# Optimization experiments

Measured on AMD Instinct MI355X. Metric: run time of the kernel, lower is better.

The kernel has to match this reference:

```python
import jax, jax.numpy as jnp
import numpy as np

B, T, D = 4096, 64, 128  # batch, n_tokens, d_model
LN_EPS = 1e-5


def setup_inputs() -> dict:
    key = jax.random.key(0)
    ks = jax.random.split(key, 3)
    X = jax.random.normal(ks[0], (B, T, D), dtype=jnp.float32)
    # torch Linear weights are (out_features, in_features)
    W1 = jax.random.normal(ks[1], (D, T * D), dtype=jnp.float32) * (T * D) ** -0.5
    b1 = jnp.zeros((D,), dtype=jnp.float32)
    W2 = jax.random.normal(ks[2], (T * D, D), dtype=jnp.float32) * D ** -0.5
    b2 = jnp.zeros((T * D,), dtype=jnp.float32)
    gamma = jnp.ones((D,), dtype=jnp.float32)
    beta = jnp.zeros((D,), dtype=jnp.float32)
    return {"X": X, "W1": W1, "b1": b1, "W2": W2, "b2": b2, "gamma": gamma, "beta": beta}


def reference(X, W1, b1, W2, b2, gamma, beta):
    b, t, d = X.shape
    scale = d ** -0.5
    # single-head self-attention with Q=K=V=X
    scores = jnp.einsum("btd,bsd->bts", X, X) * scale          # (B,T,T)
    attn = jax.nn.softmax(scores, axis=-1)
    X_dot = jnp.einsum("bts,bsd->btd", attn, X)                 # (B,T,D)
    # deep MLP over flattened tokens
    Xf = X.reshape(b, t * d)
    h = jax.nn.relu(Xf @ W1.T + b1)                             # (B,D)
    X_deep = (h @ W2.T + b2).reshape(b, t, d)                   # (B,T,D)
    # residual + LayerNorm over last dim
    y = X_dot + X_deep + X
    mu = jnp.mean(y, axis=-1, keepdims=True)
    var = jnp.mean(jnp.square(y - mu), axis=-1, keepdims=True)
    y_hat = (y - mu) * jax.lax.rsqrt(var + LN_EPS)
    return y_hat * gamma + beta
```

## Files before the change

kernel.cpp:

```cpp
#include <hip/hip_runtime.h>

#define NB 4096
#define NT 64
#define ND 128
#define NTD 8192

using bf16x8 = __attribute__((ext_vector_type(8))) short;
using s16x4  = __attribute__((ext_vector_type(4))) short;
using f32x4  = __attribute__((ext_vector_type(4))) float;

__device__ __forceinline__ short f2bf(float x) {
  union { float f; unsigned u; } v; v.f = x;
  unsigned r = (v.u + 0x7FFFu + ((v.u >> 16) & 1u)) >> 16;
  return (short)r;
}
__device__ __forceinline__ float bf2f(short h) {
  union { unsigned u; float f; } v; v.u = ((unsigned)(unsigned short)h) << 16;
  return v.f;
}

__global__ __launch_bounds__(256) void k_cvt(const float* __restrict__ W1,
                                             const float* __restrict__ W2,
                                             short* __restrict__ W1b,
                                             short* __restrict__ W2b) {
  int idx = blockIdx.x * 256 + threadIdx.x;
  const float4* src; short* dst;
  if (idx < 262144) { src = (const float4*)W1; dst = W1b; }
  else { idx -= 262144; src = (const float4*)W2; dst = W2b; }
  float4 v = src[idx];
  s16x4 p = { f2bf(v.x), f2bf(v.y), f2bf(v.z), f2bf(v.w) };
  *(s16x4*)&dst[4 * idx] = p;
}

#define LDX 136
#define LDT 72
#define LDP 72

__global__ __launch_bounds__(256) void k_attn(const float* __restrict__ X,
                                              short* __restrict__ ydot) {
  __shared__ short Xl[NT * LDX];
  __shared__ short XT[ND * LDT];
  __shared__ short Pl[4][16 * LDP];

  const int b = blockIdx.x;
  const int tid = threadIdx.x;
  const float4* X4 = (const float4*)(X + (size_t)b * NTD);

  for (int it = 0; it < 8; ++it) {
    int idx = tid + 256 * it;
    int r = idx >> 5;
    int c4 = idx & 31;
    float4 v = X4[idx];
    short h0 = f2bf(v.x), h1 = f2bf(v.y), h2 = f2bf(v.z), h3 = f2bf(v.w);
    s16x4 p = { h0, h1, h2, h3 };
    *(s16x4*)&Xl[r * LDX + 4 * c4] = p;
    int c = 4 * c4;
    XT[(c + 0) * LDT + r] = h0;
    XT[(c + 1) * LDT + r] = h1;
    XT[(c + 2) * LDT + r] = h2;
    XT[(c + 3) * LDT + r] = h3;
  }
  __syncthreads();

  const int w = tid >> 6;
  const int l = tid & 63;
  const int g = l >> 4;
  const int ln = l & 15;

  f32x4 S[4];
  for (int tj = 0; tj < 4; ++tj) S[tj] = f32x4{0.f, 0.f, 0.f, 0.f};
  for (int kk = 0; kk < 4; ++kk) {
    bf16x8 a = *(const bf16x8*)&Xl[(16 * w + ln) * LDX + 32 * kk + 8 * g];
    for (int tj = 0; tj < 4; ++tj) {
      bf16x8 bb = *(const bf16x8*)&Xl[(16 * tj + ln) * LDX + 32 * kk + 8 * g];
      S[tj] = __builtin_amdgcn_mfma_f32_16x16x32_bf16(a, bb, S[tj], 0, 0, 0);
    }
  }

  const float scale = 0.08838834764831845f;
  float li[4];
  for (int i = 0; i < 4; ++i) {
    float p[4];
    float mx = -1e30f;
    for (int tj = 0; tj < 4; ++tj) {
      float s = S[tj][i] * scale;
      p[tj] = s;
      mx = fmaxf(mx, s);
    }
    for (int msk = 1; msk < 16; msk <<= 1) mx = fmaxf(mx, __shfl_xor(mx, msk));
    float sum = 0.f;
    for (int tj = 0; tj < 4; ++tj) {
      float e = __expf(p[tj] - mx);
      p[tj] = e;
      sum += e;
    }
    for (int msk = 1; msk < 16; msk <<= 1) sum += __shfl_xor(sum, msk);
    li[i] = 1.0f / sum;
    for (int tj = 0; tj < 4; ++tj)
      Pl[w][(4 * g + i) * LDP + 16 * tj + ln] = f2bf(p[tj]);
  }
  __syncthreads();

  bf16x8 a0 = *(const bf16x8*)&Pl[w][ln * LDP + 8 * g];
  bf16x8 a1 = *(const bf16x8*)&Pl[w][ln * LDP + 32 + 8 * g];
  short* yrow = ydot + (size_t)b * NTD;
  for (int c = 0; c < 8; ++c) {
    f32x4 acc = f32x4{0.f, 0.f, 0.f, 0.f};
    bf16x8 b0 = *(const bf16x8*)&XT[(16 * c + ln) * LDT + 8 * g];
    bf16x8 b1 = *(const bf16x8*)&XT[(16 * c + ln) * LDT + 32 + 8 * g];
    acc = __builtin_amdgcn_mfma_f32_16x16x32_bf16(a0, b0, acc, 0, 0, 0);
    acc = __builtin_amdgcn_mfma_f32_16x16x32_bf16(a1, b1, acc, 0, 0, 0);
    for (int i = 0; i < 4; ++i) {
      int row = 16 * w + 4 * g + i;
      int col = 16 * c + ln;
      float y = acc[i] * li[i] + bf2f(Xl[row * LDX + col]);
      yrow[row * ND + col] = f2bf(y);
    }
  }
}

#define LDA1 40

__global__ __launch_bounds__(256) void k_gemm1(const float* __restrict__ X,
                                               const short* __restrict__ W1b,
                                               float* __restrict__ hacc) {
  __shared__ short Al[64 * LDA1];
  __shared__ short Bl[128 * LDA1];
  const int mt = blockIdx.x;
  const int kz = blockIdx.y;
  const int tid = threadIdx.x;
  const int w = tid >> 6, l = tid & 63, g = l >> 4, ln = l & 15;

  f32x4 acc[8];
  for (int c = 0; c < 8; ++c) acc[c] = f32x4{0.f, 0.f, 0.f, 0.f};

  for (int s = 0; s < 16; ++s) {
    int kb = kz * 512 + s * 32;
    for (int it = 0; it < 2; ++it) {
      int idx = tid + 256 * it;
      int r = idx >> 3, f = idx & 7;
      float4 v = ((const float4*)X)[(size_t)(mt * 64 + r) * 2048 + (kb >> 2) + f];
      s16x4 p = { f2bf(v.x), f2bf(v.y), f2bf(v.z), f2bf(v.w) };
      *(s16x4*)&Al[r * LDA1 + 4 * f] = p;
    }
    for (int it = 0; it < 2; ++it) {
      int idx = tid + 256 * it;
      int n = idx >> 2, f = idx & 3;
      bf16x8 v = *(const bf16x8*)&W1b[(size_t)n * NTD + kb + 8 * f];
      *(bf16x8*)&Bl[n * LDA1 + 8 * f] = v;
    }
    __syncthreads();
    bf16x8 a = *(const bf16x8*)&Al[(16 * w + ln) * LDA1 + 8 * g];
    for (int c = 0; c < 8; ++c) {
      bf16x8 bb = *(const bf16x8*)&Bl[(16 * c + ln) * LDA1 + 8 * g];
      acc[c] = __builtin_amdgcn_mfma_f32_16x16x32_bf16(a, bb, acc[c], 0, 0, 0);
    }
    __syncthreads();
  }
  for (int c = 0; c < 8; ++c)
    for (int i = 0; i < 4; ++i) {
      int m = mt * 64 + 16 * w + 4 * g + i;
      int n = 16 * c + ln;
      atomicAdd(&hacc[m * ND + n], acc[c][i]);
    }
}

__global__ __launch_bounds__(256) void k_hact(const float* __restrict__ hacc,
                                              const float* __restrict__ b1,
                                              short* __restrict__ hb) {
  int idx = blockIdx.x * 256 + threadIdx.x;
  float v = hacc[idx] + b1[idx & 127];
  hb[idx] = f2bf(fmaxf(v, 0.f));
}

#define LDK 136

__global__ __launch_bounds__(256) void k_gemm2(const short* __restrict__ hb,
                                               const short* __restrict__ W2b,
                                               const short* __restrict__ ydot,
                                               const float* __restrict__ b2,
                                               const float* __restrict__ gamma,
                                               const float* __restrict__ beta,
                                               float* __restrict__ out) {
  __shared__ short Al[64 * LDK];
  __shared__ short Bl[128 * LDK];
  __shared__ short Yl[64 * LDK];
  __shared__ float g_s[128], be_s[128], b2_s[128];

  const int mt = blockIdx.x, nt = blockIdx.y;
  const int tid = threadIdx.x;

  for (int it = 0; it < 4; ++it) {
    int idx = tid + 256 * it;
    int r = idx >> 4, f = idx & 15;
    *(bf16x8*)&Al[r * LDK + 8 * f] =
        *(const bf16x8*)&hb[(size_t)(mt * 64 + r) * ND + 8 * f];
  }
  for (int it = 0; it < 8; ++it) {
    int idx = tid + 256 * it;
    int n = idx >> 4, f = idx & 15;
    *(bf16x8*)&Bl[n * LDK + 8 * f] =
        *(const bf16x8*)&W2b[(size_t)(nt * 128 + n) * ND + 8 * f];
  }
  for (int it = 0; it < 4; ++it) {
    int idx = tid + 256 * it;
    int r = idx >> 4, f = idx & 15;
    *(bf16x8*)&Yl[r * LDK + 8 * f] =
        *(const bf16x8*)&ydot[(size_t)(mt * 64 + r) * NTD + nt * 128 + 8 * f];
  }
  if (tid < 128) {
    g_s[tid] = gamma[tid];
    be_s[tid] = beta[tid];
    b2_s[tid] = b2[nt * 128 + tid];
  }
  __syncthreads();

  const int w = tid >> 6, l = tid & 63, g = l >> 4, ln = l & 15;
  f32x4 acc[8];
  for (int c = 0; c < 8; ++c) acc[c] = f32x4{0.f, 0.f, 0.f, 0.f};
  for (int kk = 0; kk < 4; ++kk) {
    bf16x8 a = *(const bf16x8*)&Al[(16 * w + ln) * LDK + 32 * kk + 8 * g];
    for (int c = 0; c < 8; ++c) {
      bf16x8 bb = *(const bf16x8*)&Bl[(16 * c + ln) * LDK + 32 * kk + 8 * g];
      acc[c] = __builtin_amdgcn_mfma_f32_16x16x32_bf16(a, bb, acc[c], 0, 0, 0);
    }
  }

  for (int i = 0; i < 4; ++i) {
    int lr = 16 * w + 4 * g + i;
    float v[8];
    float s = 0.f;
    for (int c = 0; c < 8; ++c) {
      int d = 16 * c + ln;
      v[c] = acc[c][i] + b2_s[d] + bf2f(Yl[lr * LDK + d]);
      s += v[c];
    }
    for (int msk = 1; msk < 16; msk <<= 1) s += __shfl_xor(s, msk);
    float mu = s * (1.f / 128.f);
    float s2 = 0.f;
    for (int c = 0; c < 8; ++c) { float d2 = v[c] - mu; s2 += d2 * d2; }
    for (int msk = 1; msk < 16; msk <<= 1) s2 += __shfl_xor(s2, msk);
    float rstd = rsqrtf(s2 * (1.f / 128.f) + 1e-5f);
    size_t base = (size_t)(mt * 64 + lr) * NTD + (size_t)nt * 128;
    for (int c = 0; c < 8; ++c) {
      int d = 16 * c + ln;
      out[base + d] = (v[c] - mu) * rstd * g_s[d] + be_s[d];
    }
  }
}

extern "C" void kernel_launch(void* const* d_in, const int* in_sizes, int n_in,
                              void* d_out, int out_size, void* d_ws, size_t ws_size,
                              hipStream_t stream) {
  const float* X     = (const float*)d_in[0];
  const float* W1    = (const float*)d_in[1];
  const float* b1    = (const float*)d_in[2];
  const float* W2    = (const float*)d_in[3];
  const float* b2    = (const float*)d_in[4];
  const float* gamma = (const float*)d_in[5];
  const float* beta  = (const float*)d_in[6];
  float* out = (float*)d_out;

  char* ws = (char*)d_ws;
  short* ydot = (short*)ws;
  short* W1b  = (short*)(ws + 67108864);
  short* W2b  = (short*)(ws + 67108864 + 2097152);
  float* hacc = (float*)(ws + 67108864 + 2 * 2097152);
  short* hb   = (short*)(ws + 67108864 + 3 * 2097152);

  hipMemsetAsync(hacc, 0, (size_t)NB * ND * sizeof(float), stream);
  k_cvt<<<2048, 256, 0, stream>>>(W1, W2, W1b, W2b);
  k_attn<<<NB, 256, 0, stream>>>(X, ydot);
  k_gemm1<<<dim3(64, 16), 256, 0, stream>>>(X, W1b, hacc);
  k_hact<<<2048, 256, 0, stream>>>(hacc, b1, hb);
  k_gemm2<<<dim3(64, 64), 256, 0, stream>>>(hb, W2b, ydot, b2, gamma, beta, out);
}
```

Baseline: 358.7 us.

## Cache bf16 X, split-K partials without atomics, coalesce attn and output stores

The attention kernel now also writes a bf16 copy of X, which the first GEMM reads instead of re-reading and converting fp32 X. The first GEMM uses a 64-wide K step and a 4-way split-K that writes separate partial buffers, replacing the memset and the atomics; the activation kernel sums the four partials with vectorised loads. The attention transpose is built from shared memory, and both the attention output and the final LayerNorm output are staged through shared memory so global stores are coalesced and vectorised. In exchange, the first GEMM launches far fewer blocks, there are extra shared-memory round trips and barriers, and extra workspace traffic for Xbf and the partial buffers.

Measured after the change: 469.4 us. 1.31x slower.

```diff
diff --git a/kernel.cpp b/kernel.cpp
--- a/kernel.cpp
+++ b/kernel.cpp
@@ -35,9 +35,11 @@
 #define LDX 136
 #define LDT 72
 #define LDP 72
+#define LDO 136
 
 __global__ __launch_bounds__(256) void k_attn(const float* __restrict__ X,
-                                              short* __restrict__ ydot) {
+                                              short* __restrict__ ydot,
+                                              short* __restrict__ Xbf) {
   __shared__ short Xl[NT * LDX];
   __shared__ short XT[ND * LDT];
   __shared__ short Pl[4][16 * LDP];
@@ -45,20 +47,27 @@
   const int b = blockIdx.x;
   const int tid = threadIdx.x;
   const float4* X4 = (const float4*)(X + (size_t)b * NTD);
+  short* xb = Xbf + (size_t)b * NTD;
 
   for (int it = 0; it < 8; ++it) {
     int idx = tid + 256 * it;
     int r = idx >> 5;
     int c4 = idx & 31;
     float4 v = X4[idx];
-    short h0 = f2bf(v.x), h1 = f2bf(v.y), h2 = f2bf(v.z), h3 = f2bf(v.w);
-    s16x4 p = { h0, h1, h2, h3 };
+    s16x4 p = { f2bf(v.x), f2bf(v.y), f2bf(v.z), f2bf(v.w) };
     *(s16x4*)&Xl[r * LDX + 4 * c4] = p;
-    int c = 4 * c4;
-    XT[(c + 0) * LDT + r] = h0;
-    XT[(c + 1) * LDT + r] = h1;
-    XT[(c + 2) * LDT + r] = h2;
-    XT[(c + 3) * LDT + r] = h3;
+    *(s16x4*)&xb[4 * idx] = p;
+  }
+  __syncthreads();
+
+  {
+    int d = tid >> 1;
+    int t0 = (tid & 1) * 32;
+    for (int j = 0; j < 8; ++j) {
+      s16x4 p;
+      for (int e = 0; e < 4; ++e) p[e] = Xl[(t0 + 4 * j + e) * LDX + d];
+      *(s16x4*)&XT[d * LDT + t0 + 4 * j] = p;
+    }
   }
   __syncthreads();
 
@@ -99,31 +108,47 @@
     for (int tj = 0; tj < 4; ++tj)
       Pl[w][(4 * g + i) * LDP + 16 * tj + ln] = f2bf(p[tj]);
   }
-  __syncthreads();
 
   bf16x8 a0 = *(const bf16x8*)&Pl[w][ln * LDP + 8 * g];
   bf16x8 a1 = *(const bf16x8*)&Pl[w][ln * LDP + 32 + 8 * g];
-  short* yrow = ydot + (size_t)b * NTD;
+  f32x4 av[8];
   for (int c = 0; c < 8; ++c) {
     f32x4 acc = f32x4{0.f, 0.f, 0.f, 0.f};
     bf16x8 b0 = *(const bf16x8*)&XT[(16 * c + ln) * LDT + 8 * g];
     bf16x8 b1 = *(const bf16x8*)&XT[(16 * c + ln) * LDT + 32 + 8 * g];
     acc = __builtin_amdgcn_mfma_f32_16x16x32_bf16(a0, b0, acc, 0, 0, 0);
     acc = __builtin_amdgcn_mfma_f32_16x16x32_bf16(a1, b1, acc, 0, 0, 0);
+    av[c] = acc;
+  }
+  for (int c = 0; c < 8; ++c)
     for (int i = 0; i < 4; ++i) {
       int row = 16 * w + 4 * g + i;
       int col = 16 * c + ln;
-      float y = acc[i] * li[i] + bf2f(Xl[row * LDX + col]);
-      yrow[row * ND + col] = f2bf(y);
-    }
-  }
-}
-
-#define LDA1 40
-
-__global__ __launch_bounds__(256) void k_gemm1(const float* __restrict__ X,
+      av[c][i] = av[c][i] * li[i] + bf2f(Xl[row * LDX + col]);
+    }
+  __syncthreads();
+
+  short* Ol = XT;
+  for (int c = 0; c < 8; ++c)
+    for (int i = 0; i < 4; ++i) {
+      int row = 16 * w + 4 * g + i;
+      int col = 16 * c + ln;
+      Ol[row * LDO + col] = f2bf(av[c][i]);
+    }
+  __syncthreads();
+  {
+    int row = tid >> 2, seg = tid & 3;
+    short* yrow = ydot + (size_t)b * NTD + row * ND + seg * 32;
+    for (int j = 0; j < 4; ++j)
+      *(bf16x8*)&yrow[8 * j] = *(const bf16x8*)&Ol[row * LDO + seg * 32 + 8 * j];
+  }
+}
+
+#define LDA1 72
+
+__global__ __launch_bounds__(256) void k_gemm1(const short* __restrict__ Xbf,
                                                const short* __restrict__ W1b,
-                                               float* __restrict__ hacc) {
+                                               float* __restrict__ hpart) {
   __shared__ short Al[64 * LDA1];
   __shared__ short Bl[128 * LDA1];
   const int mt = blockIdx.x;
@@ -134,46 +159,59 @@
   f32x4 acc[8];
   for (int c = 0; c < 8; ++c) acc[c] = f32x4{0.f, 0.f, 0.f, 0.f};
 
-  for (int s = 0; s < 16; ++s) {
-    int kb = kz * 512 + s * 32;
+  for (int s = 0; s < 32; ++s) {
+    int kb = kz * 2048 + s * 64;
     for (int it = 0; it < 2; ++it) {
       int idx = tid + 256 * it;
       int r = idx >> 3, f = idx & 7;
-      float4 v = ((const float4*)X)[(size_t)(mt * 64 + r) * 2048 + (kb >> 2) + f];
-      s16x4 p = { f2bf(v.x), f2bf(v.y), f2bf(v.z), f2bf(v.w) };
-      *(s16x4*)&Al[r * LDA1 + 4 * f] = p;
-    }
-    for (int it = 0; it < 2; ++it) {
+      *(bf16x8*)&Al[r * LDA1 + 8 * f] =
+          *(const bf16x8*)&Xbf[(size_t)(mt * 64 + r) * NTD + kb + 8 * f];
+    }
+    for (int it = 0; it < 4; ++it) {
       int idx = tid + 256 * it;
-      int n = idx >> 2, f = idx & 3;
-      bf16x8 v = *(const bf16x8*)&W1b[(size_t)n * NTD + kb + 8 * f];
-      *(bf16x8*)&Bl[n * LDA1 + 8 * f] = v;
+      int n = idx >> 3, f = idx & 7;
+      *(bf16x8*)&Bl[n * LDA1 + 8 * f] =
+          *(const bf16x8*)&W1b[(size_t)n * NTD + kb + 8 * f];
     }
     __syncthreads();
-    bf16x8 a = *(const bf16x8*)&Al[(16 * w + ln) * LDA1 + 8 * g];
-    for (int c = 0; c < 8; ++c) {
-      bf16x8 bb = *(const bf16x8*)&Bl[(16 * c + ln) * LDA1 + 8 * g];
-      acc[c] = __builtin_amdgcn_mfma_f32_16x16x32_bf16(a, bb, acc[c], 0, 0, 0);
+    for (int kk = 0; kk < 2; ++kk) {
+      bf16x8 a = *(const bf16x8*)&Al[(16 * w + ln) * LDA1 + 32 * kk + 8 * g];
+      for (int c = 0; c < 8; ++c) {
+        bf16x8 bb = *(const bf16x8*)&Bl[(16 * c + ln) * LDA1 + 32 * kk + 8 * g];
+        acc[c] = __builtin_amdgcn_mfma_f32_16x16x32_bf16(a, bb, acc[c], 0, 0, 0);
+      }
     }
     __syncthreads();
   }
+  float* hp = hpart + (size_t)kz * (NB * ND);
   for (int c = 0; c < 8; ++c)
     for (int i = 0; i < 4; ++i) {
       int m = mt * 64 + 16 * w + 4 * g + i;
       int n = 16 * c + ln;
-      atomicAdd(&hacc[m * ND + n], acc[c][i]);
-    }
-}
-
-__global__ __launch_bounds__(256) void k_hact(const float* __restrict__ hacc,
+      hp[m * ND + n] = acc[c][i];
+    }
+}
+
+__global__ __launch_bounds__(256) void k_hact(const float* __restrict__ hpart,
                                               const float* __restrict__ b1,
                                               short* __restrict__ hb) {
   int idx = blockIdx.x * 256 + threadIdx.x;
-  float v = hacc[idx] + b1[idx & 127];
-  hb[idx] = f2bf(fmaxf(v, 0.f));
+  const float4* p0 = (const float4*)hpart;
+  float4 v = p0[idx];
+  float4 v1 = p0[idx + 131072];
+  float4 v2 = p0[idx + 262144];
+  float4 v3 = p0[idx + 393216];
+  float4 bb = ((const float4*)b1)[idx & 31];
+  s16x4 r;
+  r[0] = f2bf(fmaxf(v.x + v1.x + v2.x + v3.x + bb.x, 0.f));
+  r[1] = f2bf(fmaxf(v.y + v1.y + v2.y + v3.y + bb.y, 0.f));
+  r[2] = f2bf(fmaxf(v.z + v1.z + v2.z + v3.z + bb.z, 0.f));
+  r[3] = f2bf(fmaxf(v.w + v1.w + v2.w + v3.w + bb.w, 0.f));
+  *(s16x4*)&hb[4 * idx] = r;
 }
 
 #define LDK 136
+#define LDO2 132
 
 __global__ __launch_bounds__(256) void k_gemm2(const short* __restrict__ hb,
                                                const short* __restrict__ W2b,
@@ -226,10 +264,13 @@
     }
   }
 
+  float o[4][8];
+#pragma unroll
   for (int i = 0; i < 4; ++i) {
     int lr = 16 * w + 4 * g + i;
     float v[8];
     float s = 0.f;
+#pragma unroll
     for (int c = 0; c < 8; ++c) {
       int d = 16 * c + ln;
       v[c] = acc[c][i] + b2_s[d] + bf2f(Yl[lr * LDK + d]);
@@ -238,14 +279,31 @@
     for (int msk = 1; msk < 16; msk <<= 1) s += __shfl_xor(s, msk);
     float mu = s * (1.f / 128.f);
     float s2 = 0.f;
+#pragma unroll
     for (int c = 0; c < 8; ++c) { float d2 = v[c] - mu; s2 += d2 * d2; }
     for (int msk = 1; msk < 16; msk <<= 1) s2 += __shfl_xor(s2, msk);
     float rstd = rsqrtf(s2 * (1.f / 128.f) + 1e-5f);
-    size_t base = (size_t)(mt * 64 + lr) * NTD + (size_t)nt * 128;
+#pragma unroll
     for (int c = 0; c < 8; ++c) {
       int d = 16 * c + ln;
-      out[base + d] = (v[c] - mu) * rstd * g_s[d] + be_s[d];
-    }
+      o[i][c] = (v[c] - mu) * rstd * g_s[d] + be_s[d];
+    }
+  }
+  __syncthreads();
+
+  float* Ob = (float*)Bl;
+#pragma unroll
+  for (int i = 0; i < 4; ++i) {
+    int lr = 16 * w + 4 * g + i;
+#pragma unroll
+    for (int c = 0; c < 8; ++c) Ob[lr * LDO2 + 16 * c + ln] = o[i][c];
+  }
+  __syncthreads();
+  {
+    int row = tid >> 2, seg = tid & 3;
+    float* drow = out + (size_t)(mt * 64 + row) * NTD + nt * 128 + seg * 32;
+    for (int j = 0; j < 8; ++j)
+      *(float4*)&drow[4 * j] = *(const float4*)&Ob[row * LDO2 + seg * 32 + 4 * j];
   }
 }
 
@@ -263,15 +321,15 @@
 
   char* ws = (char*)d_ws;
   short* ydot = (short*)ws;
-  short* W1b  = (short*)(ws + 67108864);
-  short* W2b  = (short*)(ws + 67108864 + 2097152);
-  float* hacc = (float*)(ws + 67108864 + 2 * 2097152);
-  short* hb   = (short*)(ws + 67108864 + 3 * 2097152);
-
-  hipMemsetAsync(hacc, 0, (size_t)NB * ND * sizeof(float), stream);
+  short* Xbf  = (short*)(ws + (64u << 20));
+  short* W1b  = (short*)(ws + (128u << 20));
+  short* W2b  = (short*)(ws + (130u << 20));
+  float* hpart = (float*)(ws + (132u << 20));
+  short* hb   = (short*)(ws + (140u << 20));
+
   k_cvt<<<2048, 256, 0, stream>>>(W1, W2, W1b, W2b);
-  k_attn<<<NB, 256, 0, stream>>>(X, ydot);
-  k_gemm1<<<dim3(64, 16), 256, 0, stream>>>(X, W1b, hacc);
-  k_hact<<<2048, 256, 0, stream>>>(hacc, b1, hb);
+  k_attn<<<NB, 256, 0, stream>>>(X, ydot, Xbf);
+  k_gemm1<<<dim3(64, 4), 256, 0, stream>>>(Xbf, W1b, hpart);
+  k_hact<<<512, 256, 0, stream>>>(hpart, b1, hb);
   k_gemm2<<<dim3(64, 64), 256, 0, stream>>>(hb, W2b, ydot, b2, gamma, beta, out);
 }
```
